# Kernel optimization log

Measured on AMD Instinct MI355X. Metric: run time of the kernel, lower is better.

## Reference

```python
import jax, jax.numpy as jnp
import numpy as np

H_SIZE = 64  # height_pad == width_pad == 64 (power of 2, no padding needed)


def _hadamard(n):
    H = np.array([[1.0]], dtype=np.float32)
    while H.shape[0] < n:
        H = np.block([[H, H], [H, -H]])
    return jnp.asarray(H)


def setup_inputs() -> dict:
    key = jax.random.key(0)
    k1, k2, k3, k4 = jax.random.split(key, 4)
    B, C_in, C_out, P = 32, 256, 256, 2
    x = jax.random.normal(k1, (B, C_in, H_SIZE, H_SIZE), dtype=jnp.float32)
    v = jax.random.uniform(k2, (P, H_SIZE, H_SIZE), dtype=jnp.float32)
    W = jax.random.normal(k3, (P, C_out, C_in), dtype=jnp.float32) * (1.0 / np.sqrt(C_in))
    T = jax.random.uniform(k4, (P, H_SIZE, H_SIZE), dtype=jnp.float32) * 0.1
    return {"x": x, "v": v, "W": W, "T": T}


def reference(x, v, W, T):
    n = H_SIZE
    H = _hadamard(n)  # symmetric, H @ H = n * I
    # 2D WHT: apply along width then height
    f1 = jnp.einsum('bchw,wk->bchk', x, H)
    f2 = jnp.einsum('bchw,hk->bckw', f1, H)
    # per-pod: scale, 1x1 conv, soft-threshold
    f3 = v[:, None, None, :, :] * f2[None]                 # (p,b,c,h,w)
    f4 = jnp.einsum('poc,pbchw->pbohw', W, f3)             # 1x1 conv, no bias
    f5 = jnp.sign(f4) * jnp.maximum(jnp.abs(f4) - T[:, None, None, :, :], 0.0)
    f6 = f5.sum(axis=0)                                     # sum over pods
    # inverse 2D WHT (H^{-1} = H / n)
    f7 = jnp.einsum('bchw,wk->bchk', f6, H) / n
    f8 = jnp.einsum('bchw,hk->bckw', f7, H) / n
    return f8 + x  # residual
```

## Files before the change

### kernel.cpp

```cpp
#include <hip/hip_runtime.h>
#include <stdint.h>


typedef __attribute__((ext_vector_type(4))) float f32x4_t;
typedef __attribute__((ext_vector_type(8))) __bf16 bf16x8_t;
typedef __attribute__((ext_vector_type(8))) unsigned short u16x8_t;
typedef __attribute__((ext_vector_type(4))) unsigned short u16x4_t;
typedef __attribute__((ext_vector_type(4))) unsigned int u32x4_t;

__device__ __forceinline__ float bf2f(unsigned short u) {
  union { unsigned int i; float f; } x; x.i = ((unsigned int)u) << 16; return x.f;
}
__device__ __forceinline__ unsigned short f2bf(float f) {
  union { float f; unsigned int i; } x; x.f = f;
  unsigned int i = x.i;
  return (unsigned short)((i + 0x7FFFu + ((i >> 16) & 1u)) >> 16);
}
__device__ __forceinline__ unsigned short f2bf_t(float f) {
  union { float f; unsigned int i; } x; x.f = f;
  return (unsigned short)(x.i >> 16);
}
__device__ __forceinline__ size_t Faddr(size_t f) {
  return ((f >> 12) << 13) + 4096 + (f & 4095);
}

__global__ __launch_bounds__(512) void k_fwd(const float* __restrict__ x,
                                             unsigned short* __restrict__ obuf) {
  __shared__ unsigned short smem[36864];
  int tid = threadIdx.x;
  int lane = tid & 63, wave = tid >> 6;
  int quad = lane >> 4, l15 = lane & 15;
  int cg = blockIdx.x, b = blockIdx.y;
  size_t img = (size_t)b * 256 + cg * 8 + wave;
  unsigned short* T1t = smem + wave * 4608;

  const float* xim = x + img * 4096;
#pragma unroll
  for (int l = 0; l < 16; l++) {
    int e = (l * 64 + lane) * 4;
    f32x4_t sv = *(const f32x4_t*)(xim + e);
    u16x4_t u;
#pragma unroll
    for (int j = 0; j < 4; j++) u[j] = f2bf_t(sv[j]);
    int row = e >> 6, col = e & 63;
    *(u16x4_t*)&T1t[row * 72 + col] = u;
  }

  bf16x8_t hf[2][4];
#pragma unroll
  for (int kc = 0; kc < 2; kc++)
#pragma unroll
    for (int t = 0; t < 4; t++) {
      bf16x8_t h;
#pragma unroll
      for (int j = 0; j < 8; j++) {
        int k = kc * 32 + quad * 8 + j, n = t * 16 + l15;
        h[j] = (__builtin_popcount(k & n) & 1) ? (__bf16)-1.0f : (__bf16)1.0f;
      }
      hf[kc][t] = h;
    }

  bf16x8_t xa[4][2];
#pragma unroll
  for (int mt = 0; mt < 4; mt++)
#pragma unroll
    for (int kc = 0; kc < 2; kc++)
      xa[mt][kc] = *(const bf16x8_t*)&T1t[(mt * 16 + l15) * 72 + kc * 32 + quad * 8];

#pragma unroll
  for (int nt = 0; nt < 4; nt++) {
    f32x4_t a1c[4];
#pragma unroll
    for (int mt = 0; mt < 4; mt++) a1c[mt] = (f32x4_t){0.f, 0.f, 0.f, 0.f};
#pragma unroll
    for (int kc = 0; kc < 2; kc++)
#pragma unroll
      for (int mt = 0; mt < 4; mt++)
        a1c[mt] = __builtin_amdgcn_mfma_f32_16x16x32_bf16(xa[mt][kc], hf[kc][nt], a1c[mt], 0, 0, 0);
#pragma unroll
    for (int mt = 0; mt < 4; mt++) {
      u16x4_t t4;
#pragma unroll
      for (int r = 0; r < 4; r++) t4[r] = f2bf_t(a1c[mt][r]);
      *(u16x4_t*)&T1t[(nt * 16 + l15) * 72 + mt * 16 + quad * 4] = t4;
    }
  }

  f32x4_t acc[4][4];
#pragma unroll
  for (int mt = 0; mt < 4; mt++)
#pragma unroll
    for (int nt = 0; nt < 4; nt++) acc[mt][nt] = (f32x4_t){0.f, 0.f, 0.f, 0.f};
#pragma unroll
  for (int kc = 0; kc < 2; kc++)
#pragma unroll
    for (int nt = 0; nt < 4; nt++) {
      bf16x8_t bfr = *(bf16x8_t*)&T1t[(nt * 16 + l15) * 72 + kc * 32 + quad * 8];
#pragma unroll
      for (int mt = 0; mt < 4; mt++)
        acc[mt][nt] = __builtin_amdgcn_mfma_f32_16x16x32_bf16(hf[kc][mt], bfr, acc[mt][nt], 0, 0, 0);
    }

  __syncthreads();
#pragma unroll
  for (int mt = 0; mt < 4; mt++)
#pragma unroll
    for (int nt = 0; nt < 4; nt++)
#pragma unroll
      for (int r = 0; r < 4; r++) {
        int pos = (mt * 16 + quad * 4 + r) * 64 + nt * 16 + l15;
        smem[pos * 8 + (wave ^ (quad << 1))] = f2bf(acc[mt][nt][r]);
      }
  __syncthreads();
  size_t fbase = ((size_t)b * 32 + cg) * 4096;
  int hb = wave >> 2;
  if (hb) {
#pragma unroll
    for (int i = 0; i < 8; i++) {
      int pos = i * 512 + tid;
      u32x4_t c = *(u32x4_t*)&smem[pos * 8];
      const int q = (2 * i + 1) & 3;
      u32x4_t o;
      o[0] = c[0 ^ q]; o[1] = c[1 ^ q]; o[2] = c[2 ^ q]; o[3] = c[3 ^ q];
      *(u32x4_t*)(obuf + Faddr((fbase + pos) * 8)) = o;
    }
  } else {
#pragma unroll
    for (int i = 0; i < 8; i++) {
      int pos = i * 512 + tid;
      u32x4_t c = *(u32x4_t*)&smem[pos * 8];
      const int q = (2 * i) & 3;
      u32x4_t o;
      o[0] = c[0 ^ q]; o[1] = c[1 ^ q]; o[2] = c[2 ^ q]; o[3] = c[3 ^ q];
      *(u32x4_t*)(obuf + Faddr((fbase + pos) * 8)) = o;
    }
  }
}

__global__ __launch_bounds__(256) void k_gemm(const float* __restrict__ Wf,
                                              const float* __restrict__ vv,
                                              const float* __restrict__ TT,
                                              unsigned short* __restrict__ obuf) {
  __shared__ unsigned short smem2[24576];
  unsigned short* Alds = smem2;
  int tid = threadIdx.x;
  int lane = tid & 63, wave = tid >> 6;
  int quad = lane >> 4, l15 = lane & 15;
  int wm = wave & 1, wn = wave >> 1;
  int n0 = blockIdx.x * 128;
  int m0 = blockIdx.y * 128;
  int b  = blockIdx.z;

  f32x4_t acc[4][4];
#pragma unroll
  for (int mt = 0; mt < 4; mt++)
#pragma unroll
    for (int nt = 0; nt < 4; nt++) acc[mt][nt] = (f32x4_t){0.f, 0.f, 0.f, 0.f};

  auto issueB = [&](int ks, int buf) {
    unsigned short* Bl = smem2 + 8192 + buf * 8192;
#pragma unroll
    for (int i = 0; i < 4; i++) {
      int idx = i * 256 + tid;
      int r = idx & 127, cch = idx >> 7;
      size_t f = (((size_t)b * 32 + ks * 8 + cch) * 4096 + n0 + r) * 8;
      const unsigned short* src = obuf + Faddr(f);
      __builtin_amdgcn_global_load_lds(
          (const __attribute__((address_space(1))) void*)src,
          (__attribute__((address_space(3))) void*)(Bl + idx * 8), 16, 0, 0);
    }
  };
  auto fetchA = [&](int ks, f32x4_t (&ar)[4][2]) {
    int k0 = ks * 64;
#pragma unroll
    for (int i = 0; i < 4; i++) {
      int idx = i * 256 + tid;
      int r = idx >> 3, cch = idx & 7;
      int gch = cch ^ (r & 7);
      int m = m0 + r;
      const float* wp = Wf + ((m & 1) << 16) + ((m >> 1) << 8) + k0 + gch * 8;
      ar[i][0] = *(const f32x4_t*)wp;
      ar[i][1] = *(const f32x4_t*)(wp + 4);
    }
  };
  auto writeA = [&](f32x4_t (&ar)[4][2]) {
#pragma unroll
    for (int i = 0; i < 4; i++) {
      int idx = i * 256 + tid;
      u16x8_t u;
#pragma unroll
      for (int j = 0; j < 4; j++) { u[j] = f2bf_t(ar[i][0][j]); u[4 + j] = f2bf_t(ar[i][1][j]); }
      *(u16x8_t*)&Alds[idx * 8] = u;
    }
  };

  f32x4_t areg[4][2];
  issueB(0, 0);
  fetchA(0, areg);
  writeA(areg);
  __syncthreads();

  for (int ks = 0; ks < 4; ++ks) {
    int p = ks & 1;
    if (ks < 3) {
      issueB(ks + 1, p ^ 1);
      fetchA(ks + 1, areg);
    }
    unsigned short* Bl = smem2 + 8192 + p * 8192;
#pragma unroll
    for (int kk = 0; kk < 2; ++kk) {
      bf16x8_t af[4], bfr[4];
#pragma unroll
      for (int mt = 0; mt < 4; mt++) {
        int row = wm * 64 + mt * 16 + l15;
        int s = (kk * 4 + quad) ^ (row & 7);
        af[mt] = *(const bf16x8_t*)&Alds[row * 64 + s * 8];
      }
      int ch = kk * 4 + quad;
#pragma unroll
      for (int nt = 0; nt < 4; nt++)
        bfr[nt] = *(const bf16x8_t*)&Bl[ch * 1024 + (wn * 64 + nt * 16 + l15) * 8];
#pragma unroll
      for (int mt = 0; mt < 4; mt++)
#pragma unroll
        for (int nt = 0; nt < 4; nt++)
          acc[mt][nt] = __builtin_amdgcn_mfma_f32_16x16x32_bf16(af[mt], bfr[nt], acc[mt][nt], 0, 0, 0);
    }
    __syncthreads();
    if (ks < 3) {
      writeA(areg);
      __syncthreads();
    }
  }

#pragma unroll
  for (int nt = 0; nt < 4; nt++) {
    int posl = wn * 64 + nt * 16 + l15;
    int pos = n0 + posl;
    float v0 = vv[pos], v1 = vv[4096 + pos];
    float t0 = TT[pos], t1 = TT[4096 + pos];
#pragma unroll
    for (int mt = 0; mt < 4; mt++)
#pragma unroll
      for (int rp = 0; rp < 2; rp++) {
        int ol = wm * 32 + mt * 8 + quad * 2 + rp;
        float z0 = acc[mt][nt][rp * 2 + 0] * v0;
        float z1 = acc[mt][nt][rp * 2 + 1] * v1;
        float s0 = copysignf(fmaxf(fabsf(z0) - t0, 0.f), z0);
        float s1 = copysignf(fmaxf(fabsf(z1) - t1, 0.f), z1);
        smem2[ol * 136 + posl] = f2bf(s0 + s1);
      }
  }
  __syncthreads();
  int o0 = m0 >> 1;
#pragma unroll
  for (int i = 0; i < 4; i++) {
    int ci = i * 256 + tid;
    int row = ci >> 4, cc = ci & 15;
    u16x8_t vch = *(u16x8_t*)&smem2[row * 136 + cc * 8];
    size_t img = (size_t)b * 256 + o0 + row;
    *(u16x8_t*)(obuf + img * 8192 + n0 + cc * 8) = vch;
  }
}

__global__ __launch_bounds__(256) void k_inv(const float* __restrict__ x,
                                             unsigned short* __restrict__ obuf) {
  __shared__ unsigned short smem[18432];
  int tid = threadIdx.x;
  int lane = tid & 63, wave = tid >> 6;
  int quad = lane >> 4, l15 = lane & 15;
  size_t img = (size_t)blockIdx.x * 4 + wave;
  unsigned short* T1t = smem + wave * 4608;

#pragma unroll
  for (int l = 0; l < 8; l++) {
    int e = (l * 64 + lane) * 8;
    u16x8_t sv = *(const u16x8_t*)(obuf + img * 8192 + e);
    int row = e >> 6, col = e & 63;
    *(u16x8_t*)&T1t[row * 72 + col] = sv;
  }

  bf16x8_t hf[2][4];
#pragma unroll
  for (int kc = 0; kc < 2; kc++)
#pragma unroll
    for (int t = 0; t < 4; t++) {
      bf16x8_t h;
#pragma unroll
      for (int j = 0; j < 8; j++) {
        int k = kc * 32 + quad * 8 + j, n = t * 16 + l15;
        h[j] = (__builtin_popcount(k & n) & 1) ? (__bf16)-1.0f : (__bf16)1.0f;
      }
      hf[kc][t] = h;
    }

  bf16x8_t fa[4][2];
#pragma unroll
  for (int mt = 0; mt < 4; mt++)
#pragma unroll
    for (int kc = 0; kc < 2; kc++)
      fa[mt][kc] = *(const bf16x8_t*)&T1t[(mt * 16 + l15) * 72 + kc * 32 + quad * 8];

#pragma unroll
  for (int nt = 0; nt < 4; nt++) {
    f32x4_t a1c[4];
#pragma unroll
    for (int mt = 0; mt < 4; mt++) a1c[mt] = (f32x4_t){0.f, 0.f, 0.f, 0.f};
#pragma unroll
    for (int kc = 0; kc < 2; kc++)
#pragma unroll
      for (int mt = 0; mt < 4; mt++)
        a1c[mt] = __builtin_amdgcn_mfma_f32_16x16x32_bf16(fa[mt][kc], hf[kc][nt], a1c[mt], 0, 0, 0);
#pragma unroll
    for (int mt = 0; mt < 4; mt++) {
      u16x4_t t4;
#pragma unroll
      for (int r = 0; r < 4; r++) t4[r] = f2bf_t(a1c[mt][r]);
      *(u16x4_t*)&T1t[(nt * 16 + l15) * 72 + mt * 16 + quad * 4] = t4;
    }
  }

  f32x4_t acc[4][4];
#pragma unroll
  for (int mt = 0; mt < 4; mt++)
#pragma unroll
    for (int nt = 0; nt < 4; nt++) acc[mt][nt] = (f32x4_t){0.f, 0.f, 0.f, 0.f};
#pragma unroll
  for (int kc = 0; kc < 2; kc++)
#pragma unroll
    for (int nt = 0; nt < 4; nt++) {
      bf16x8_t bfr = *(bf16x8_t*)&T1t[(nt * 16 + l15) * 72 + kc * 32 + quad * 8];
#pragma unroll
      for (int mt = 0; mt < 4; mt++)
        acc[mt][nt] = __builtin_amdgcn_mfma_f32_16x16x32_bf16(hf[kc][mt], bfr, acc[mt][nt], 0, 0, 0);
    }

  const float sc = 1.0f / 4096.0f;
#pragma unroll
  for (int mt = 0; mt < 4; mt++)
#pragma unroll
    for (int nt = 0; nt < 4; nt++)
#pragma unroll
      for (int r = 0; r < 4; r++)
        T1t[(mt * 16 + quad * 4 + r) * 72 + nt * 16 + l15] = f2bf(acc[mt][nt][r] * sc);

  float* outf = (float*)obuf;
  const float* xim = x + img * 4096;
#pragma unroll
  for (int l = 0; l < 8; l++) {
    int e = (l * 64 + lane) * 8;
    int row = e >> 6, col = e & 63;
    u16x8_t tv = *(u16x8_t*)&T1t[row * 72 + col];
    f32x4_t x0 = *(const f32x4_t*)(xim + e);
    f32x4_t x1 = *(const f32x4_t*)(xim + e + 4);
    f32x4_t o0, o1;
#pragma unroll
    for (int j = 0; j < 4; j++) { o0[j] = bf2f(tv[j]) + x0[j]; o1[j] = bf2f(tv[4 + j]) + x1[j]; }
    *(f32x4_t*)(outf + img * 4096 + e) = o0;
    *(f32x4_t*)(outf + img * 4096 + e + 4) = o1;
  }
}

extern "C" void kernel_launch(void* const* d_in, const int* in_sizes, int n_in,
                              void* d_out, int out_size, void* d_ws, size_t ws_size,
                              hipStream_t stream) {
  const float* x = (const float*)d_in[0];
  const float* v = (const float*)d_in[1];
  const float* W = (const float*)d_in[2];
  const float* T = (const float*)d_in[3];
  unsigned short* obuf = (unsigned short*)d_out;
  (void)d_ws; (void)ws_size; (void)in_sizes; (void)n_in; (void)out_size;

  k_fwd<<<dim3(32, 32), 512, 0, stream>>>(x, obuf);
  k_gemm<<<dim3(32, 4, 32), 256, 0, stream>>>(W, v, T, obuf);
  k_inv<<<2048, 256, 0, stream>>>(x, obuf);
}
```

Before: 334.3 us.

## Fuse forward WHT, pod GEMM and inverse WHT into one cooperative kernel

```diff
diff --git a/kernel.cpp b/kernel.cpp
--- a/kernel.cpp
+++ b/kernel.cpp
@@ -1,6 +1,9 @@
 #include <hip/hip_runtime.h>
+#include <hip/hip_cooperative_groups.h>
 #include <stdint.h>
 
+
+namespace cgrp = cooperative_groups;
 
 typedef __attribute__((ext_vector_type(4))) float f32x4_t;
 typedef __attribute__((ext_vector_type(8))) __bf16 bf16x8_t;
@@ -23,6 +26,354 @@
 __device__ __forceinline__ size_t Faddr(size_t f) {
   return ((f >> 12) << 13) + 4096 + (f & 4095);
 }
+
+__global__ __launch_bounds__(512, 2) void k_fused(
+    const float* __restrict__ x, const float* __restrict__ Wf,
+    const float* __restrict__ vv, const float* __restrict__ TT,
+    unsigned short* __restrict__ obuf) {
+  __shared__ unsigned short smem[36864];
+  cgrp::grid_group gg = cgrp::this_grid();
+  const int tid = threadIdx.x;
+  const int lane = tid & 63, wave = tid >> 6;
+  const int quad = lane >> 4, l15 = lane & 15;
+  const int bid = blockIdx.x;
+
+  {
+    bf16x8_t hf[2][4];
+#pragma unroll
+    for (int kc = 0; kc < 2; kc++)
+#pragma unroll
+      for (int t = 0; t < 4; t++) {
+        bf16x8_t h;
+#pragma unroll
+        for (int j = 0; j < 8; j++) {
+          int k = kc * 32 + quad * 8 + j, n = t * 16 + l15;
+          h[j] = (__builtin_popcount(k & n) & 1) ? (__bf16)-1.0f : (__bf16)1.0f;
+        }
+        hf[kc][t] = h;
+      }
+
+    for (int j = 0; j < 4; ++j) {
+      __syncthreads();
+      int u = bid + j * 256;
+      int cgi = u & 31, b = u >> 5;
+      size_t img = (size_t)b * 256 + cgi * 8 + wave;
+      unsigned short* T1t = smem + wave * 4608;
+
+      const float* xim = x + img * 4096;
+#pragma unroll
+      for (int l = 0; l < 16; l++) {
+        int e = (l * 64 + lane) * 4;
+        f32x4_t sv = *(const f32x4_t*)(xim + e);
+        u16x4_t uu;
+#pragma unroll
+        for (int jj = 0; jj < 4; jj++) uu[jj] = f2bf_t(sv[jj]);
+        int row = e >> 6, col = e & 63;
+        *(u16x4_t*)&T1t[row * 72 + col] = uu;
+      }
+
+      bf16x8_t xa[4][2];
+#pragma unroll
+      for (int mt = 0; mt < 4; mt++)
+#pragma unroll
+        for (int kc = 0; kc < 2; kc++)
+          xa[mt][kc] = *(const bf16x8_t*)&T1t[(mt * 16 + l15) * 72 + kc * 32 + quad * 8];
+
+#pragma unroll
+      for (int nt = 0; nt < 4; nt++) {
+        f32x4_t a1c[4];
+#pragma unroll
+        for (int mt = 0; mt < 4; mt++) a1c[mt] = (f32x4_t){0.f, 0.f, 0.f, 0.f};
+#pragma unroll
+        for (int kc = 0; kc < 2; kc++)
+#pragma unroll
+          for (int mt = 0; mt < 4; mt++)
+            a1c[mt] = __builtin_amdgcn_mfma_f32_16x16x32_bf16(xa[mt][kc], hf[kc][nt], a1c[mt], 0, 0, 0);
+#pragma unroll
+        for (int mt = 0; mt < 4; mt++) {
+          u16x4_t t4;
+#pragma unroll
+          for (int r = 0; r < 4; r++) t4[r] = f2bf_t(a1c[mt][r]);
+          *(u16x4_t*)&T1t[(nt * 16 + l15) * 72 + mt * 16 + quad * 4] = t4;
+        }
+      }
+
+      f32x4_t acc[4][4];
+#pragma unroll
+      for (int mt = 0; mt < 4; mt++)
+#pragma unroll
+        for (int nt = 0; nt < 4; nt++) acc[mt][nt] = (f32x4_t){0.f, 0.f, 0.f, 0.f};
+#pragma unroll
+      for (int kc = 0; kc < 2; kc++)
+#pragma unroll
+        for (int nt = 0; nt < 4; nt++) {
+          bf16x8_t bfr = *(bf16x8_t*)&T1t[(nt * 16 + l15) * 72 + kc * 32 + quad * 8];
+#pragma unroll
+          for (int mt = 0; mt < 4; mt++)
+            acc[mt][nt] = __builtin_amdgcn_mfma_f32_16x16x32_bf16(hf[kc][mt], bfr, acc[mt][nt], 0, 0, 0);
+        }
+
+      __syncthreads();
+#pragma unroll
+      for (int mt = 0; mt < 4; mt++)
+#pragma unroll
+        for (int nt = 0; nt < 4; nt++)
+#pragma unroll
+          for (int r = 0; r < 4; r++) {
+            int pos = (mt * 16 + quad * 4 + r) * 64 + nt * 16 + l15;
+            smem[pos * 8 + (wave ^ (quad << 1))] = f2bf(acc[mt][nt][r]);
+          }
+      __syncthreads();
+      size_t fbase = ((size_t)b * 32 + cgi) * 4096;
+      int hb = wave >> 2;
+      if (hb) {
+#pragma unroll
+        for (int i = 0; i < 8; i++) {
+          int pos = i * 512 + tid;
+          u32x4_t c = *(u32x4_t*)&smem[pos * 8];
+          const int q = (2 * i + 1) & 3;
+          u32x4_t o;
+          o[0] = c[0 ^ q]; o[1] = c[1 ^ q]; o[2] = c[2 ^ q]; o[3] = c[3 ^ q];
+          *(u32x4_t*)(obuf + Faddr((fbase + pos) * 8)) = o;
+        }
+      } else {
+#pragma unroll
+        for (int i = 0; i < 8; i++) {
+          int pos = i * 512 + tid;
+          u32x4_t c = *(u32x4_t*)&smem[pos * 8];
+          const int q = (2 * i) & 3;
+          u32x4_t o;
+          o[0] = c[0 ^ q]; o[1] = c[1 ^ q]; o[2] = c[2 ^ q]; o[3] = c[3 ^ q];
+          *(u32x4_t*)(obuf + Faddr((fbase + pos) * 8)) = o;
+        }
+      }
+    }
+  }
+
+  gg.sync();
+
+  {
+    const int wm = wave & 3, wn = wave >> 2;
+    for (int j = 0; j < 8; ++j) {
+      __syncthreads();
+      int u = bid + j * 256;
+      int n0 = (u & 31) * 128;
+      int m0 = ((u >> 5) & 1) * 256;
+      int b  = u >> 6;
+
+      f32x4_t acc[4][4];
+#pragma unroll
+      for (int mt = 0; mt < 4; mt++)
+#pragma unroll
+        for (int nt = 0; nt < 4; nt++) acc[mt][nt] = (f32x4_t){0.f, 0.f, 0.f, 0.f};
+
+      auto issueB = [&](int ks, int buf) {
+        unsigned short* Bl = smem + 16384 + buf * 8192;
+#pragma unroll
+        for (int i = 0; i < 2; i++) {
+          int idx = i * 512 + tid;
+          int r = idx & 127, cch = idx >> 7;
+          size_t f = (((size_t)b * 32 + ks * 8 + cch) * 4096 + n0 + r) * 8;
+          const unsigned short* src = obuf + Faddr(f);
+          __builtin_amdgcn_global_load_lds(
+              (const __attribute__((address_space(1))) void*)src,
+              (__attribute__((address_space(3))) void*)(Bl + idx * 8), 16, 0, 0);
+        }
+      };
+      auto fetchA = [&](int ks, f32x4_t (&ar)[4][2]) {
+        int k0 = ks * 64;
+#pragma unroll
+        for (int i = 0; i < 4; i++) {
+          int idx = i * 512 + tid;
+          int r = idx >> 3, cch = idx & 7;
+          int gch = cch ^ (r & 7);
+          int m = m0 + r;
+          const float* wp = Wf + ((m & 1) << 16) + ((m >> 1) << 8) + k0 + gch * 8;
+          ar[i][0] = *(const f32x4_t*)wp;
+          ar[i][1] = *(const f32x4_t*)(wp + 4);
+        }
+      };
+      auto writeA = [&](f32x4_t (&ar)[4][2]) {
+#pragma unroll
+        for (int i = 0; i < 4; i++) {
+          int idx = i * 512 + tid;
+          u16x8_t uu;
+#pragma unroll
+          for (int jj = 0; jj < 4; jj++) { uu[jj] = f2bf_t(ar[i][0][jj]); uu[4 + jj] = f2bf_t(ar[i][1][jj]); }
+          *(u16x8_t*)&smem[idx * 8] = uu;
+        }
+      };
+
+      f32x4_t areg[4][2];
+      issueB(0, 0);
+      fetchA(0, areg);
+      writeA(areg);
+      __syncthreads();
+
+      for (int ks = 0; ks < 4; ++ks) {
+        int p = ks & 1;
+        if (ks < 3) {
+          issueB(ks + 1, p ^ 1);
+          fetchA(ks + 1, areg);
+        }
+        unsigned short* Bl = smem + 16384 + p * 8192;
+#pragma unroll
+        for (int kk = 0; kk < 2; ++kk) {
+          bf16x8_t af[4], bfr[4];
+#pragma unroll
+          for (int mt = 0; mt < 4; mt++) {
+            int row = wm * 64 + mt * 16 + l15;
+            int s = (kk * 4 + quad) ^ (row & 7);
+            af[mt] = *(const bf16x8_t*)&smem[row * 64 + s * 8];
+          }
+          int ch = kk * 4 + quad;
+#pragma unroll
+          for (int nt = 0; nt < 4; nt++)
+            bfr[nt] = *(const bf16x8_t*)&Bl[ch * 1024 + (wn * 64 + nt * 16 + l15) * 8];
+#pragma unroll
+          for (int mt = 0; mt < 4; mt++)
+#pragma unroll
+            for (int nt = 0; nt < 4; nt++)
+              acc[mt][nt] = __builtin_amdgcn_mfma_f32_16x16x32_bf16(af[mt], bfr[nt], acc[mt][nt], 0, 0, 0);
+        }
+        __syncthreads();
+        if (ks < 3) {
+          writeA(areg);
+          __syncthreads();
+        }
+      }
+
+#pragma unroll
+      for (int nt = 0; nt < 4; nt++) {
+        int posl = wn * 64 + nt * 16 + l15;
+        int pos = n0 + posl;
+        float v0 = vv[pos], v1 = vv[4096 + pos];
+        float t0 = TT[pos], t1 = TT[4096 + pos];
+#pragma unroll
+        for (int mt = 0; mt < 4; mt++)
+#pragma unroll
+          for (int rp = 0; rp < 2; rp++) {
+            int ol = wm * 32 + mt * 8 + quad * 2 + rp;
+            float z0 = acc[mt][nt][rp * 2 + 0] * v0;
+            float z1 = acc[mt][nt][rp * 2 + 1] * v1;
+            float s0 = copysignf(fmaxf(fabsf(z0) - t0, 0.f), z0);
+            float s1 = copysignf(fmaxf(fabsf(z1) - t1, 0.f), z1);
+            smem[ol * 136 + posl] = f2bf(s0 + s1);
+          }
+      }
+      __syncthreads();
+      int o0 = m0 >> 1;
+#pragma unroll
+      for (int i = 0; i < 4; i++) {
+        int ci = i * 512 + tid;
+        int row = ci >> 4, cc = ci & 15;
+        u16x8_t vch = *(u16x8_t*)&smem[row * 136 + cc * 8];
+        size_t img = (size_t)b * 256 + o0 + row;
+        *(u16x8_t*)(obuf + img * 8192 + n0 + cc * 8) = vch;
+      }
+    }
+  }
+
+  gg.sync();
+
+  {
+    bf16x8_t hf[2][4];
+#pragma unroll
+    for (int kc = 0; kc < 2; kc++)
+#pragma unroll
+      for (int t = 0; t < 4; t++) {
+        bf16x8_t h;
+#pragma unroll
+        for (int jj = 0; jj < 8; jj++) {
+          int k = kc * 32 + quad * 8 + jj, n = t * 16 + l15;
+          h[jj] = (__builtin_popcount(k & n) & 1) ? (__bf16)-1.0f : (__bf16)1.0f;
+        }
+        hf[kc][t] = h;
+      }
+
+    for (int j = 0; j < 4; ++j) {
+      __syncthreads();
+      int u = bid + j * 256;
+      size_t img = (size_t)u * 8 + wave;
+      unsigned short* T1t = smem + wave * 4608;
+
+#pragma unroll
+      for (int l = 0; l < 8; l++) {
+        int e = (l * 64 + lane) * 8;
+        u16x8_t sv = *(const u16x8_t*)(obuf + img * 8192 + e);
+        int row = e >> 6, col = e & 63;
+        *(u16x8_t*)&T1t[row * 72 + col] = sv;
+      }
+
+      bf16x8_t fa[4][2];
+#pragma unroll
+      for (int mt = 0; mt < 4; mt++)
+#pragma unroll
+        for (int kc = 0; kc < 2; kc++)
+          fa[mt][kc] = *(const bf16x8_t*)&T1t[(mt * 16 + l15) * 72 + kc * 32 + quad * 8];
+
+#pragma unroll
+      for (int nt = 0; nt < 4; nt++) {
+        f32x4_t a1c[4];
+#pragma unroll
+        for (int mt = 0; mt < 4; mt++) a1c[mt] = (f32x4_t){0.f, 0.f, 0.f, 0.f};
+#pragma unroll
+        for (int kc = 0; kc < 2; kc++)
+#pragma unroll
+          for (int mt = 0; mt < 4; mt++)
+            a1c[mt] = __builtin_amdgcn_mfma_f32_16x16x32_bf16(fa[mt][kc], hf[kc][nt], a1c[mt], 0, 0, 0);
+#pragma unroll
+        for (int mt = 0; mt < 4; mt++) {
+          u16x4_t t4;
+#pragma unroll
+          for (int r = 0; r < 4; r++) t4[r] = f2bf_t(a1c[mt][r]);
+          *(u16x4_t*)&T1t[(nt * 16 + l15) * 72 + mt * 16 + quad * 4] = t4;
+        }
+      }
+
+      f32x4_t acc[4][4];
+#pragma unroll
+      for (int mt = 0; mt < 4; mt++)
+#pragma unroll
+        for (int nt = 0; nt < 4; nt++) acc[mt][nt] = (f32x4_t){0.f, 0.f, 0.f, 0.f};
+#pragma unroll
+      for (int kc = 0; kc < 2; kc++)
+#pragma unroll
+        for (int nt = 0; nt < 4; nt++) {
+          bf16x8_t bfr = *(bf16x8_t*)&T1t[(nt * 16 + l15) * 72 + kc * 32 + quad * 8];
+#pragma unroll
+          for (int mt = 0; mt < 4; mt++)
+            acc[mt][nt] = __builtin_amdgcn_mfma_f32_16x16x32_bf16(hf[kc][mt], bfr, acc[mt][nt], 0, 0, 0);
+        }
+
+      const float sc = 1.0f / 4096.0f;
+#pragma unroll
+      for (int mt = 0; mt < 4; mt++)
+#pragma unroll
+        for (int nt = 0; nt < 4; nt++)
+#pragma unroll
+          for (int r = 0; r < 4; r++)
+            T1t[(mt * 16 + quad * 4 + r) * 72 + nt * 16 + l15] = f2bf(acc[mt][nt][r] * sc);
+
+      float* outf = (float*)obuf;
+      const float* xim = x + img * 4096;
+#pragma unroll
+      for (int l = 0; l < 8; l++) {
+        int e = (l * 64 + lane) * 8;
+        int row = e >> 6, col = e & 63;
+        u16x8_t tv = *(u16x8_t*)&T1t[row * 72 + col];
+        f32x4_t x0 = *(const f32x4_t*)(xim + e);
+        f32x4_t x1 = *(const f32x4_t*)(xim + e + 4);
+        f32x4_t o0, o1;
+#pragma unroll
+        for (int jj = 0; jj < 4; jj++) { o0[jj] = bf2f(tv[jj]) + x0[jj]; o1[jj] = bf2f(tv[4 + jj]) + x1[jj]; }
+        *(f32x4_t*)(outf + img * 4096 + e) = o0;
+        *(f32x4_t*)(outf + img * 4096 + e + 4) = o1;
+      }
+    }
+  }
+}
+
 
 __global__ __launch_bounds__(512) void k_fwd(const float* __restrict__ x,
                                              unsigned short* __restrict__ obuf) {
@@ -371,7 +722,12 @@
   unsigned short* obuf = (unsigned short*)d_out;
   (void)d_ws; (void)ws_size; (void)in_sizes; (void)n_in; (void)out_size;
 
-  k_fwd<<<dim3(32, 32), 512, 0, stream>>>(x, obuf);
-  k_gemm<<<dim3(32, 4, 32), 256, 0, stream>>>(W, v, T, obuf);
-  k_inv<<<2048, 256, 0, stream>>>(x, obuf);
-}
+  void* args[] = {(void*)&x, (void*)&W, (void*)&v, (void*)&T, (void*)&obuf};
+  hipError_t e = hipLaunchCooperativeKernel((const void*)k_fused, dim3(256),
+                                            dim3(512), args, 0, stream);
+  if (e != hipSuccess) {
+    k_fwd<<<dim3(32, 32), 512, 0, stream>>>(x, obuf);
+    k_gemm<<<dim3(32, 4, 32), 256, 0, stream>>>(W, v, T, obuf);
+    k_inv<<<2048, 256, 0, stream>>>(x, obuf);
+  }
+}
```

After: 436.8 us. 30.7% more time.
